# Performance work log

Measured on AMD Instinct MI355X. Metric: run time of the kernel, lower is better.

The kernel has to match this reference:

```python
import jax, jax.numpy as jnp
import numpy as np

B, S, E, P, K, H = 32, 512, 1024, 256, 3, 8
KERNELS = 4  # conv repeated KERNELS times then averaged -> identical to a single conv


def setup_inputs() -> dict:
    key = jax.random.key(0)
    ks = jax.random.split(key, 8)
    sc = 0.02
    x = jax.random.normal(ks[0], (B, S, E), jnp.float32)
    # lengths must satisfy 3 <= l <= S-1 so slice [1:l+1] and conv length l-2 are valid
    seq_length = jax.random.randint(ks[1], (B,), 16, S - 1)
    proj_w = jax.random.normal(ks[2], (E, P), jnp.float32) * sc
    proj_b = jnp.zeros((P,), jnp.float32)
    conv_w = jax.random.normal(ks[3], (P, P, K), jnp.float32) * sc  # (out, in, width)
    conv_b = jnp.zeros((P,), jnp.float32)
    attn_w = jax.random.normal(ks[4], (P, H * S), jnp.float32) * sc
    attn_b = jnp.zeros((H * S,), jnp.float32)
    c1_w = jax.random.normal(ks[5], (P, P // 2), jnp.float32) * sc
    c1_b = jnp.zeros((P // 2,), jnp.float32)
    c2_w = jax.random.normal(ks[6], (P // 2, 2), jnp.float32) * sc
    c2_b = jnp.zeros((2,), jnp.float32)
    return dict(x=x, seq_length=seq_length, proj_w=proj_w, proj_b=proj_b,
                conv_w=conv_w, conv_b=conv_b, attn_w=attn_w, attn_b=attn_b,
                c1_w=c1_w, c1_b=c1_b, c2_w=c2_w, c2_b=c2_b)


def _forward(x, seq_length, proj_w, proj_b, conv_w, conv_b, attn_w, attn_b,
             c1_w, c1_b, c2_w, c2_b):
    # projection: (B,S,E) -> (B,S,P)
    proj = jnp.einsum('bse,ep->bsp', x, proj_w) + proj_b
    proj_pc = jnp.transpose(proj, (0, 2, 1))  # (B,P,S)
    # original convs each sample over slice [1:l+1]; conv is local, so conv the
    # full slice [1:] once and mask invalid tail positions per sample.
    conv = jax.lax.conv_general_dilated(
        proj_pc[:, :, 1:], conv_w, window_strides=(1,), padding='VALID',
        dimension_numbers=('NCH', 'OIH', 'NCH'))  # (B,P,S-K)
    conv = jax.nn.relu(conv + conv_b[None, :, None])
    # sum of KERNELS identical relu(conv) outputs divided by KERNELS == conv (identity)
    m = S - K  # conv output length over slice [1:]
    l = seq_length[:, None]  # (B,1)
    valid = jnp.arange(m)[None, :] < (l - (K - 1))  # output j valid iff j < l-2
    conv = jnp.where(valid[:, None, :], conv, 0.0)
    # pad: position 0 zero, conv outputs at 1..l-2, zeros after -> (B,P,S)
    rep_conv = jnp.zeros((B, P, S), conv.dtype).at[:, :, 1:1 + m].set(conv)
    rep_conv = jnp.transpose(rep_conv, (0, 2, 1))  # (B,S,P)
    # attention: logits (B,S,H*S), softmax over the FULL H*S axis (original dim=1)
    logits = jnp.einsum('bsp,pk->bsk', rep_conv, attn_w) + attn_b
    attn = jax.nn.softmax(logits, axis=-1).reshape(B, S, H, S)
    # per sample: mean over heads, sum over query rows -> weights over key pos q
    w = attn.sum(axis=(1, 2)) / H  # (B,S)
    rep_attn = jnp.einsum('bq,bqp->bp', w, rep_conv)  # (B,P)
    h = jnp.einsum('bp,ph->bh', rep_attn, c1_w) + c1_b
    h = jnp.where(h > 0, h, 0.01 * h)  # LeakyReLU(0.01)
    cls = jnp.einsum('bh,hc->bc', h, c2_w) + c2_b
    return jax.nn.softmax(cls, axis=-1)


def reference(x, seq_length, proj_w, proj_b, conv_w, conv_b, attn_w, attn_b,
              c1_w, c1_b, c2_w, c2_b):
    probs = _forward(x, seq_length, proj_w, proj_b, conv_w, conv_b,
                     attn_w, attn_b, c1_w, c1_b, c2_w, c2_b)
    return probs, jnp.argmax(probs, axis=1)
```

## Files before the change

### kernel.cpp

```cpp
#include <hip/hip_runtime.h>
#include <hip/hip_fp8.h>

#define B_ 32
#define S_ 512
#define E_ 1024
#define P_ 256
#define HH 8

typedef __attribute__((ext_vector_type(8))) short bf16x8;
typedef __attribute__((ext_vector_type(8))) unsigned short us8;
typedef __attribute__((ext_vector_type(4))) unsigned short us4;
typedef __attribute__((ext_vector_type(16))) float f32x16;
typedef __attribute__((ext_vector_type(4))) float f32x4;
typedef __attribute__((ext_vector_type(8))) unsigned char u8x8;

#define SA 8.0f
#define SB 16.0f
#define SINV (1.0f / 128.0f)

static __device__ __forceinline__ unsigned short f2bf(float f) {
  union { float f; unsigned int u; } v;
  v.f = f;
  unsigned int r = (v.u + 0x7FFFu + ((v.u >> 16) & 1u)) >> 16;
  return (unsigned short)r;
}
static __device__ __forceinline__ float bf2f(unsigned short u) {
  union { unsigned int u; float f; } v;
  v.u = ((unsigned int)u) << 16;
  return v.f;
}
static __device__ __forceinline__ unsigned char f2fp8(float f) {
  return (unsigned char)__hip_cvt_float_to_fp8(f, __HIP_SATFINITE, __HIP_E4M3);
}

__global__ __launch_bounds__(256) void k_prep(const float* __restrict__ pw,
                                              const float* __restrict__ cw,
                                              const float* __restrict__ aw,
                                              unsigned short* __restrict__ pwB,
                                              unsigned short* __restrict__ wtB,
                                              unsigned char* __restrict__ awB8,
                                              float* __restrict__ zbase) {
  int bid = blockIdx.x;
  int t = threadIdx.x;
  if (bid < 160) {
    zbase[bid * 256 + t] = 0.f;
    return;
  }
  bid -= 160;
  if (bid < 128) {
    int g = bid >> 4, kc = (bid & 15) * 4 + (t >> 6);
    int l = t & 63;
    int n = g * 32 + (l & 31);
    int kbase = kc * 16 + (l >> 5) * 8;
    us8 v;
#pragma unroll
    for (int j = 0; j < 8; j++) v[j] = f2bf(pw[(size_t)(kbase + j) * P_ + n]);
    *(us8*)(pwB + ((size_t)g * 64 + kc) * 512 + l * 8) = v;
    return;
  }
  bid -= 128;
  if (bid < 96) {
    int g = bid / 12, kidx = (bid % 12) * 4 + (t >> 6);
    int l = t & 63;
    int o = g * 32 + (l & 31);
    int xb = kidx * 16 + (l >> 5) * 8;
    us8 v;
#pragma unroll
    for (int j = 0; j < 8; j++) {
      int x = xb + j;
      int k = x >> 8, i = x & 255;
      v[j] = f2bf(cw[(size_t)o * 768 + i * 3 + k]);
    }
    *(us8*)(wtB + ((size_t)g * 48 + kidx) * 512 + l * 8) = v;
    return;
  }
  bid -= 96;
  {
    int g = bid >> 1, ks = (bid & 1) * 4 + (t >> 6);
    int l = t & 63;
    int j0 = g * 16 + (l & 15);
    int kbase = ks * 32 + (l >> 4) * 8;
    u8x8 v;
#pragma unroll
    for (int j = 0; j < 8; j++) v[j] = f2fp8(aw[(size_t)(kbase + j) * 4096 + j0] * SB);
    *(u8x8*)(awB8 + ((size_t)g * 8 + ks) * 512 + l * 8) = v;
  }
}

__global__ __launch_bounds__(256) void k_swz8(const unsigned short* __restrict__ src,
                                              unsigned char* __restrict__ dst) {
  int g = blockIdx.x, ks = blockIdx.y * 4 + (threadIdx.x >> 6);
  int l = threadIdx.x & 63;
  us8 v = *(const us8*)(src + (size_t)(g * 16 + (l & 15)) * 256 + ks * 32 + (l >> 4) * 8);
  u8x8 o;
#pragma unroll
  for (int j = 0; j < 8; j++) o[j] = f2fp8(bf2f(v[j]) * SA);
  *(u8x8*)(dst + ((size_t)g * 8 + ks) * 512 + l * 8) = o;
}

__global__ __launch_bounds__(512) void k_proj_mfma(const float* __restrict__ x,
                                                   const unsigned short* __restrict__ pwB,
                                                   const float* __restrict__ pb,
                                                   unsigned short* __restrict__ proj16) {
  __shared__ unsigned short As[16 * 64 * 8];
  const int m0 = blockIdx.x * 64;
  const int t = threadIdx.x;
  const int w = t >> 6, lane = t & 63, ln31 = lane & 31, kh = lane >> 5;
  const int c0 = w * 32;

  f32x16 acc0, acc1;
#pragma unroll
  for (int r = 0; r < 16; r++) { acc0[r] = 0.f; acc1[r] = 0.f; }

  const unsigned short* bp = pwB + (size_t)w * 64 * 512 + lane * 8;

  for (int kc = 0; kc < E_; kc += 128) {
#pragma unroll
    for (int i = 0; i < 4; i++) {
      int c = t + i * 512;
      int row = c >> 5, pos = c & 31;
      float4 v = *(const float4*)(x + (size_t)(m0 + row) * E_ + kc + pos * 4);
      us4 h;
      h[0] = f2bf(v.x); h[1] = f2bf(v.y); h[2] = f2bf(v.z); h[3] = f2bf(v.w);
      *(us4*)&As[((pos >> 1) * 64 + row) * 8 + (pos & 1) * 4] = h;
    }
    __syncthreads();
    const int kcs = kc >> 4;
#pragma unroll
    for (int kk = 0; kk < 8; kk++) {
      bf16x8 a0 = *(const bf16x8*)&As[((2 * kk + kh) * 64 + ln31) * 8];
      bf16x8 a1 = *(const bf16x8*)&As[((2 * kk + kh) * 64 + 32 + ln31) * 8];
      bf16x8 b  = *(const bf16x8*)(bp + (size_t)(kcs + kk) * 512);
      acc0 = __builtin_amdgcn_mfma_f32_32x32x16_bf16(a0, b, acc0, 0, 0, 0);
      acc1 = __builtin_amdgcn_mfma_f32_32x32x16_bf16(a1, b, acc1, 0, 0, 0);
    }
    __syncthreads();
  }
  float pbv = pb[c0 + ln31];
#pragma unroll
  for (int r = 0; r < 16; r++) {
    int rl = (r & 3) + 8 * (r >> 2) + 4 * kh;
    proj16[(size_t)(m0 + rl) * P_ + c0 + ln31]      = f2bf(acc0[r] + pbv);
    proj16[(size_t)(m0 + 32 + rl) * P_ + c0 + ln31] = f2bf(acc1[r] + pbv);
  }
}

__global__ __launch_bounds__(512) void k_conv_mfma(const unsigned short* __restrict__ proj16,
                                                   const unsigned short* __restrict__ wtB,
                                                   const float* __restrict__ cb,
                                                   const int* __restrict__ seq,
                                                   unsigned short* __restrict__ rep16) {
  __shared__ unsigned short As[32 * 66 * 8];
  const int m0 = blockIdx.x * 64;
  const int bb = m0 >> 9, s0 = m0 & 511;
  const int t = threadIdx.x;
  const int w = t >> 6, lane = t & 63, ln31 = lane & 31, kh = lane >> 5;
  const int c0 = w * 32;

#pragma unroll
  for (int i = 0; i < 5; i++) {
    int c = t + i * 512;
    if (c < 2112) {
      int row = c >> 5, kk2 = c & 31;
      us8 v = {0, 0, 0, 0, 0, 0, 0, 0};
      if (s0 + row <= 511)
        v = *(const us8*)(proj16 + (size_t)(bb * S_ + s0 + row) * P_ + kk2 * 8);
      *(us8*)&As[(kk2 * 66 + row) * 8] = v;
    }
  }
  __syncthreads();

  f32x16 acc0, acc1;
#pragma unroll
  for (int r = 0; r < 16; r++) { acc0[r] = 0.f; acc1[r] = 0.f; }

  const unsigned short* bbase = wtB + (size_t)w * 48 * 512 + lane * 8;

#pragma unroll
  for (int k = 0; k < 3; k++) {
#pragma unroll
    for (int kk = 0; kk < 16; kk++) {
      bf16x8 a0 = *(const bf16x8*)&As[((2 * kk + kh) * 66 + k + ln31) * 8];
      bf16x8 a1 = *(const bf16x8*)&As[((2 * kk + kh) * 66 + k + 32 + ln31) * 8];
      bf16x8 b  = *(const bf16x8*)(bbase + (size_t)(k * 16 + kk) * 512);
      acc0 = __builtin_amdgcn_mfma_f32_32x32x16_bf16(a0, b, acc0, 0, 0, 0);
      acc1 = __builtin_amdgcn_mfma_f32_32x32x16_bf16(a1, b, acc1, 0, 0, 0);
    }
  }

  int l = seq[bb];
  float cbv = cb[c0 + ln31];
#pragma unroll
  for (int r = 0; r < 16; r++) {
    int rl = (r & 3) + 8 * (r >> 2) + 4 * kh;
    int s_a = s0 + rl, s_b = s0 + 32 + rl;
    float ma = (s_a >= 1 && s_a <= 509 && s_a < l - 1) ? 1.f : 0.f;
    float mb = (s_b >= 1 && s_b <= 509 && s_b < l - 1) ? 1.f : 0.f;
    rep16[(size_t)(m0 + rl) * P_ + c0 + ln31]      = f2bf(fmaxf(acc0[r] + cbv, 0.f) * ma);
    rep16[(size_t)(m0 + 32 + rl) * P_ + c0 + ln31] = f2bf(fmaxf(acc1[r] + cbv, 0.f) * mb);
  }
}

__global__ __launch_bounds__(256, 2) void k_attn_mfma(const unsigned char* __restrict__ repF8,
                                                      const unsigned char* __restrict__ awB8,
                                                      const float* __restrict__ ab,
                                                      unsigned short* __restrict__ E16,
                                                      float* __restrict__ Z) {
  const int m0 = blockIdx.x * 64;
  const int q0 = blockIdx.y * 128;
  const int t = threadIdx.x;
  const int w = t >> 6, lane = t & 63;
  const int ln15 = lane & 15, l4 = lane >> 4;

  long ar[4][8];
  {
    const unsigned char* abase = repF8 + (size_t)(m0 >> 4) * 8 * 512 + lane * 8;
#pragma unroll
    for (int rt = 0; rt < 4; rt++)
#pragma unroll
      for (int ks = 0; ks < 8; ks++)
        ar[rt][ks] = *(const long*)(abase + (size_t)(rt * 8 + ks) * 512);
  }

  const int qg = (q0 >> 5) + w;

  f32x4 ef[8];
#pragma unroll
  for (int i = 0; i < 8; i++) ef[i] = (f32x4){0.f, 0.f, 0.f, 0.f};

#pragma unroll 1
  for (int h = 0; h < HH; h++) {
    const unsigned char* bh = awB8 + (size_t)(h * 32 + qg * 2) * 8 * 512 + lane * 8;
    f32x4 acc[8];
#pragma unroll
    for (int i = 0; i < 8; i++) acc[i] = (f32x4){0.f, 0.f, 0.f, 0.f};
#pragma unroll
    for (int ks = 0; ks < 8; ks++) {
      long b0 = *(const long*)(bh + (size_t)ks * 512);
      long b1 = *(const long*)(bh + (size_t)(8 + ks) * 512);
#pragma unroll
      for (int rt = 0; rt < 4; rt++) {
        acc[rt * 2 + 0] = __builtin_amdgcn_mfma_f32_16x16x32_fp8_fp8(ar[rt][ks], b0, acc[rt * 2 + 0], 0, 0, 0);
        acc[rt * 2 + 1] = __builtin_amdgcn_mfma_f32_16x16x32_fp8_fp8(ar[rt][ks], b1, acc[rt * 2 + 1], 0, 0, 0);
      }
    }
    float bias0 = ab[h * 512 + qg * 32 + ln15];
    float bias1 = ab[h * 512 + qg * 32 + 16 + ln15];
#pragma unroll
    for (int rt = 0; rt < 4; rt++)
#pragma unroll
      for (int r = 0; r < 4; r++) {
        ef[rt * 2 + 0][r] += __expf(acc[rt * 2 + 0][r] * SINV + bias0);
        ef[rt * 2 + 1][r] += __expf(acc[rt * 2 + 1][r] * SINV + bias1);
      }
  }

#pragma unroll
  for (int rt = 0; rt < 4; rt++)
#pragma unroll
    for (int r = 0; r < 4; r++) {
      int row = m0 + rt * 16 + l4 * 4 + r;
      E16[(size_t)row * 512 + qg * 32 + ln15]      = f2bf(ef[rt * 2 + 0][r]);
      E16[(size_t)row * 512 + qg * 32 + 16 + ln15] = f2bf(ef[rt * 2 + 1][r]);
    }

#pragma unroll
  for (int rt = 0; rt < 4; rt++)
#pragma unroll
    for (int r = 0; r < 4; r++) {
      float z = ef[rt * 2 + 0][r] + ef[rt * 2 + 1][r];
#pragma unroll
      for (int st = 8; st >= 1; st >>= 1) z += __shfl_xor(z, st, 64);
      if (ln15 == 0) atomicAdd(&Z[m0 + rt * 16 + l4 * 4 + r], z);
    }
}

__global__ __launch_bounds__(512) void k_w(const unsigned short* __restrict__ E16,
                                           const float* __restrict__ Z,
                                           float* __restrict__ wB) {
  __shared__ float rZ[64];
  int b = blockIdx.x, c = blockIdx.y, t = threadIdx.x;
  int s0 = c * 64;
  if (t < 64) rZ[t] = 1.0f / Z[b * 512 + s0 + t];
  __syncthreads();
  float acc = 0.f;
#pragma unroll 8
  for (int s = 0; s < 64; s++)
    acc += bf2f(E16[(size_t)(b * 512 + s0 + s) * 512 + t]) * rZ[s];
  atomicAdd(&wB[b * 512 + t], acc * (1.0f / HH));
}

__global__ __launch_bounds__(256) void k_final_a(const unsigned short* __restrict__ rep16,
                                                 const float* __restrict__ wB,
                                                 float* __restrict__ repA) {
  __shared__ float wS[64];
  int b = blockIdx.x, qc = blockIdx.y, t = threadIdx.x;
  if (t < 64) wS[t] = wB[b * 512 + qc * 64 + t];
  __syncthreads();
  int p0 = (t & 63) * 4, qo = t >> 6;
  float a0 = 0.f, a1 = 0.f, a2 = 0.f, a3 = 0.f;
  for (int q = qo; q < 64; q += 4) {
    us4 v = *(const us4*)(rep16 + (size_t)(b * 512 + qc * 64 + q) * 256 + p0);
    float wq = wS[q];
    a0 += wq * bf2f(v[0]); a1 += wq * bf2f(v[1]);
    a2 += wq * bf2f(v[2]); a3 += wq * bf2f(v[3]);
  }
  atomicAdd(&repA[b * 256 + p0 + 0], a0);
  atomicAdd(&repA[b * 256 + p0 + 1], a1);
  atomicAdd(&repA[b * 256 + p0 + 2], a2);
  atomicAdd(&repA[b * 256 + p0 + 3], a3);
}

__global__ __launch_bounds__(128) void k_final_b(const float* __restrict__ repA,
                                                 const float* __restrict__ c1w,
                                                 const float* __restrict__ c1b,
                                                 const float* __restrict__ c2w,
                                                 const float* __restrict__ c2b,
                                                 float* __restrict__ out) {
  __shared__ float hS[128];
  __shared__ float clsS[2];
  int b = blockIdx.x, t = threadIdx.x;
  float acc = c1b[t];
  for (int p = 0; p < 256; p++) acc += repA[b * 256 + p] * c1w[p * 128 + t];
  hS[t] = acc > 0.f ? acc : 0.01f * acc;
  __syncthreads();
  if (t < 2) {
    float a2 = c2b[t];
    for (int j = 0; j < 128; j++) a2 += hS[j] * c2w[j * 2 + t];
    clsS[t] = a2;
  }
  __syncthreads();
  if (t == 0) {
    float c0 = clsS[0], c1 = clsS[1];
    float m = fmaxf(c0, c1);
    float e0 = __expf(c0 - m), e1 = __expf(c1 - m);
    float inv = 1.0f / (e0 + e1);
    float p0 = e0 * inv, p1 = e1 * inv;
    out[b * 2 + 0] = p0;
    out[b * 2 + 1] = p1;
    out[B_ * 2 + b] = (p1 > p0) ? 1.0f : 0.0f;
  }
}

extern "C" void kernel_launch(void* const* d_in, const int* in_sizes, int n_in,
                              void* d_out, int out_size, void* d_ws, size_t ws_size,
                              hipStream_t stream) {
  const float* x   = (const float*)d_in[0];
  const int*   seq = (const int*)d_in[1];
  const float* pw  = (const float*)d_in[2];
  const float* pb  = (const float*)d_in[3];
  const float* cw  = (const float*)d_in[4];
  const float* cb  = (const float*)d_in[5];
  const float* aw  = (const float*)d_in[6];
  const float* ab  = (const float*)d_in[7];
  const float* c1w = (const float*)d_in[8];
  const float* c1b = (const float*)d_in[9];
  const float* c2w = (const float*)d_in[10];
  const float* c2b = (const float*)d_in[11];
  float* out = (float*)d_out;

  char* ws = (char*)d_ws;
  unsigned short* proj16 = (unsigned short*)(ws);
  unsigned short* E16    = (unsigned short*)(ws);
  unsigned short* rep16  = (unsigned short*)(ws + (size_t)16777216);
  unsigned char*  repF8  = (unsigned char*)(ws + (size_t)25165824);
  unsigned char*  awB8   = (unsigned char*)(ws + (size_t)29360128);
  unsigned short* pwB    = (unsigned short*)(ws + (size_t)30408704);
  unsigned short* wtB    = (unsigned short*)(ws + (size_t)30932992);
  float*          Z      = (float*)(ws + (size_t)31326208);
  float*          wB     = (float*)(ws + (size_t)31391744);
  float*          repA   = (float*)(ws + (size_t)31457280);

  k_prep<<<896, 256, 0, stream>>>(pw, cw, aw, pwB, wtB, awB8, Z);
  k_proj_mfma<<<256, 512, 0, stream>>>(x, pwB, pb, proj16);
  k_conv_mfma<<<256, 512, 0, stream>>>(proj16, wtB, cb, seq, rep16);
  k_swz8<<<dim3(1024, 2), 256, 0, stream>>>(rep16, repF8);
  k_attn_mfma<<<dim3(256, 4), 256, 0, stream>>>(repF8, awB8, ab, E16, Z);
  k_w<<<dim3(32, 8), 512, 0, stream>>>(E16, Z, wB);
  k_final_a<<<dim3(32, 8), 256, 0, stream>>>(rep16, wB, repA);
  k_final_b<<<32, 128, 0, stream>>>(repA, c1w, c1b, c2w, c2b, out);
}
```

Baseline: 214.7 us.

## Fuse attention softmax normalization and weight reduction into one kernel

The attention kernel now launches one 1024-thread block per 64-row tile, so all 512 key columns for those rows are handled in a single block. This lets the softmax denominator be reduced in shared memory and the normalized weights be accumulated straight into wB. The separate k_w kernel and the bf16 E16 intermediate it read back from global memory are removed. The A operand is staged once through LDS and shared by 16 waves instead of each wave loading it into registers, and exp is computed as exp2 with log2e folded into the scale and bias. The risks are lower occupancy with 1024-thread blocks and LDS read traffic inside the MFMA loop.

```diff
diff --git a/kernel.cpp b/kernel.cpp
--- a/kernel.cpp
+++ b/kernel.cpp
@@ -17,6 +17,8 @@
 #define SA 8.0f
 #define SB 16.0f
 #define SINV (1.0f / 128.0f)
+#define LOG2E 1.44269504088896f
+#define SINV2 (SINV * LOG2E)
 
 static __device__ __forceinline__ unsigned short f2bf(float f) {
   union { float f; unsigned int u; } v;
@@ -42,11 +44,11 @@
                                               float* __restrict__ zbase) {
   int bid = blockIdx.x;
   int t = threadIdx.x;
-  if (bid < 160) {
+  if (bid < 96) {
     zbase[bid * 256 + t] = 0.f;
     return;
   }
-  bid -= 160;
+  bid -= 96;
   if (bid < 128) {
     int g = bid >> 4, kc = (bid & 15) * 4 + (t >> 6);
     int l = t & 63;
@@ -201,28 +203,23 @@
   }
 }
 
-__global__ __launch_bounds__(256, 2) void k_attn_mfma(const unsigned char* __restrict__ repF8,
-                                                      const unsigned char* __restrict__ awB8,
-                                                      const float* __restrict__ ab,
-                                                      unsigned short* __restrict__ E16,
-                                                      float* __restrict__ Z) {
+__global__ __launch_bounds__(1024, 4) void k_attn_fused(const unsigned char* __restrict__ repF8,
+                                                        const unsigned char* __restrict__ awB8,
+                                                        const float* __restrict__ ab,
+                                                        float* __restrict__ wB) {
+  __shared__ __align__(16) unsigned char As8[16384];
+  __shared__ float zred[16][64];
+  __shared__ float rZ[64];
+
   const int m0 = blockIdx.x * 64;
-  const int q0 = blockIdx.y * 128;
+  const int b  = m0 >> 9;
   const int t = threadIdx.x;
-  const int w = t >> 6, lane = t & 63;
+  const int qg = t >> 6;
+  const int lane = t & 63;
   const int ln15 = lane & 15, l4 = lane >> 4;
 
-  long ar[4][8];
-  {
-    const unsigned char* abase = repF8 + (size_t)(m0 >> 4) * 8 * 512 + lane * 8;
-#pragma unroll
-    for (int rt = 0; rt < 4; rt++)
-#pragma unroll
-      for (int ks = 0; ks < 8; ks++)
-        ar[rt][ks] = *(const long*)(abase + (size_t)(rt * 8 + ks) * 512);
-  }
-
-  const int qg = (q0 >> 5) + w;
+  ((float4*)As8)[t] = ((const float4*)(repF8 + (size_t)m0 * 256))[t];
+  __syncthreads();
 
   f32x4 ef[8];
 #pragma unroll
@@ -240,54 +237,65 @@
       long b1 = *(const long*)(bh + (size_t)(8 + ks) * 512);
 #pragma unroll
       for (int rt = 0; rt < 4; rt++) {
-        acc[rt * 2 + 0] = __builtin_amdgcn_mfma_f32_16x16x32_fp8_fp8(ar[rt][ks], b0, acc[rt * 2 + 0], 0, 0, 0);
-        acc[rt * 2 + 1] = __builtin_amdgcn_mfma_f32_16x16x32_fp8_fp8(ar[rt][ks], b1, acc[rt * 2 + 1], 0, 0, 0);
+        long a = *(const long*)&As8[(rt * 8 + ks) * 512 + lane * 8];
+        acc[rt * 2 + 0] = __builtin_amdgcn_mfma_f32_16x16x32_fp8_fp8(a, b0, acc[rt * 2 + 0], 0, 0, 0);
+        acc[rt * 2 + 1] = __builtin_amdgcn_mfma_f32_16x16x32_fp8_fp8(a, b1, acc[rt * 2 + 1], 0, 0, 0);
       }
     }
-    float bias0 = ab[h * 512 + qg * 32 + ln15];
-    float bias1 = ab[h * 512 + qg * 32 + 16 + ln15];
+    float bias0 = ab[h * 512 + qg * 32 + ln15] * LOG2E;
+    float bias1 = ab[h * 512 + qg * 32 + 16 + ln15] * LOG2E;
 #pragma unroll
     for (int rt = 0; rt < 4; rt++)
 #pragma unroll
       for (int r = 0; r < 4; r++) {
-        ef[rt * 2 + 0][r] += __expf(acc[rt * 2 + 0][r] * SINV + bias0);
-        ef[rt * 2 + 1][r] += __expf(acc[rt * 2 + 1][r] * SINV + bias1);
+        ef[rt * 2 + 0][r] += __builtin_amdgcn_exp2f(acc[rt * 2 + 0][r] * SINV2 + bias0);
+        ef[rt * 2 + 1][r] += __builtin_amdgcn_exp2f(acc[rt * 2 + 1][r] * SINV2 + bias1);
       }
   }
 
-#pragma unroll
-  for (int rt = 0; rt < 4; rt++)
-#pragma unroll
-    for (int r = 0; r < 4; r++) {
-      int row = m0 + rt * 16 + l4 * 4 + r;
-      E16[(size_t)row * 512 + qg * 32 + ln15]      = f2bf(ef[rt * 2 + 0][r]);
-      E16[(size_t)row * 512 + qg * 32 + 16 + ln15] = f2bf(ef[rt * 2 + 1][r]);
-    }
-
+  float zr[4][4];
 #pragma unroll
   for (int rt = 0; rt < 4; rt++)
 #pragma unroll
     for (int r = 0; r < 4; r++) {
       float z = ef[rt * 2 + 0][r] + ef[rt * 2 + 1][r];
-#pragma unroll
-      for (int st = 8; st >= 1; st >>= 1) z += __shfl_xor(z, st, 64);
-      if (ln15 == 0) atomicAdd(&Z[m0 + rt * 16 + l4 * 4 + r], z);
-    }
-}
-
-__global__ __launch_bounds__(512) void k_w(const unsigned short* __restrict__ E16,
-                                           const float* __restrict__ Z,
-                                           float* __restrict__ wB) {
-  __shared__ float rZ[64];
-  int b = blockIdx.x, c = blockIdx.y, t = threadIdx.x;
-  int s0 = c * 64;
-  if (t < 64) rZ[t] = 1.0f / Z[b * 512 + s0 + t];
-  __syncthreads();
-  float acc = 0.f;
-#pragma unroll 8
-  for (int s = 0; s < 64; s++)
-    acc += bf2f(E16[(size_t)(b * 512 + s0 + s) * 512 + t]) * rZ[s];
-  atomicAdd(&wB[b * 512 + t], acc * (1.0f / HH));
+      z += __shfl_xor(z, 1);
+      z += __shfl_xor(z, 2);
+      z += __shfl_xor(z, 4);
+      z += __shfl_xor(z, 8);
+      zr[rt][r] = z;
+    }
+  if (ln15 == 0) {
+#pragma unroll
+    for (int rt = 0; rt < 4; rt++)
+#pragma unroll
+      for (int r = 0; r < 4; r++)
+        zred[qg][rt * 16 + l4 * 4 + r] = zr[rt][r];
+  }
+  __syncthreads();
+  if (t < 64) {
+    float s = 0.f;
+#pragma unroll
+    for (int ww = 0; ww < 16; ww++) s += zred[ww][t];
+    rZ[t] = 1.0f / s;
+  }
+  __syncthreads();
+
+  float w0 = 0.f, w1 = 0.f;
+#pragma unroll
+  for (int rt = 0; rt < 4; rt++)
+#pragma unroll
+    for (int r = 0; r < 4; r++) {
+      float rz = rZ[rt * 16 + l4 * 4 + r];
+      w0 += ef[rt * 2 + 0][r] * rz;
+      w1 += ef[rt * 2 + 1][r] * rz;
+    }
+  w0 += __shfl_xor(w0, 16); w0 += __shfl_xor(w0, 32);
+  w1 += __shfl_xor(w1, 16); w1 += __shfl_xor(w1, 32);
+  if (l4 == 0) {
+    atomicAdd(&wB[b * 512 + qg * 32 + ln15],      w0 * (1.0f / HH));
+    atomicAdd(&wB[b * 512 + qg * 32 + 16 + ln15], w1 * (1.0f / HH));
+  }
 }
 
 __global__ __launch_bounds__(256) void k_final_a(const unsigned short* __restrict__ rep16,
@@ -361,22 +369,19 @@
 
   char* ws = (char*)d_ws;
   unsigned short* proj16 = (unsigned short*)(ws);
-  unsigned short* E16    = (unsigned short*)(ws);
-  unsigned short* rep16  = (unsigned short*)(ws + (size_t)16777216);
-  unsigned char*  repF8  = (unsigned char*)(ws + (size_t)25165824);
-  unsigned char*  awB8   = (unsigned char*)(ws + (size_t)29360128);
-  unsigned short* pwB    = (unsigned short*)(ws + (size_t)30408704);
-  unsigned short* wtB    = (unsigned short*)(ws + (size_t)30932992);
-  float*          Z      = (float*)(ws + (size_t)31326208);
-  float*          wB     = (float*)(ws + (size_t)31391744);
-  float*          repA   = (float*)(ws + (size_t)31457280);
-
-  k_prep<<<896, 256, 0, stream>>>(pw, cw, aw, pwB, wtB, awB8, Z);
+  unsigned short* rep16  = (unsigned short*)(ws + (size_t)8388608);
+  unsigned char*  repF8  = (unsigned char*)(ws + (size_t)16777216);
+  unsigned char*  awB8   = (unsigned char*)(ws + (size_t)20971520);
+  unsigned short* pwB    = (unsigned short*)(ws + (size_t)22020096);
+  unsigned short* wtB    = (unsigned short*)(ws + (size_t)22544384);
+  float*          wB     = (float*)(ws + (size_t)22937600);
+  float*          repA   = (float*)(ws + (size_t)23003136);
+
+  k_prep<<<832, 256, 0, stream>>>(pw, cw, aw, pwB, wtB, awB8, wB);
   k_proj_mfma<<<256, 512, 0, stream>>>(x, pwB, pb, proj16);
   k_conv_mfma<<<256, 512, 0, stream>>>(proj16, wtB, cb, seq, rep16);
   k_swz8<<<dim3(1024, 2), 256, 0, stream>>>(rep16, repF8);
-  k_attn_mfma<<<dim3(256, 4), 256, 0, stream>>>(repF8, awB8, ab, E16, Z);
-  k_w<<<dim3(32, 8), 512, 0, stream>>>(E16, Z, wB);
+  k_attn_fused<<<256, 1024, 0, stream>>>(repF8, awB8, ab, wB);
   k_final_a<<<dim3(32, 8), 256, 0, stream>>>(rep16, wB, repA);
   k_final_b<<<32, 128, 0, stream>>>(repA, c1w, c1b, c2w, c2b, out);
 }
```

Measured after the change: 243.0 us. 13.2% more time.
